# Kernel optimization log

Measured on AMD Instinct MI355X. Metric: run time of the kernel, lower is better.

The kernel has to match this reference:

```python
import jax, jax.numpy as jnp
import numpy as np

D_MODEL = 192
DEPTH = 12
D_INNER = 2 * D_MODEL          # 384
D_STATE = 16
D_CONV = 4
DT_RANK = (D_MODEL + 15) // 16  # 12
T_FRAMES = 8
PATCH = 16
IMG = 224
BATCH = 2
NUM_CLASSES = 1000
EPS = 1e-5


def setup_inputs() -> dict:
    key = jax.random.key(0)
    it = iter(jax.random.split(key, 64))
    def rn(shape, s=0.02):
        return jax.random.normal(next(it), shape, jnp.float32) * s
    inp = {
        'x': jax.random.normal(next(it), (BATCH, 3, T_FRAMES, IMG, IMG), jnp.float32),
        'patch_w': rn((D_MODEL, 3, PATCH, PATCH)),
        'patch_b': jnp.zeros((D_MODEL,), jnp.float32),
        'cls_token': rn((1, 1, D_MODEL)),
        'pos_embed': rn((1, (IMG // PATCH) ** 2 + 1, D_MODEL)),
        'temporal_pos': rn((1, T_FRAMES, D_MODEL)),
        'norm_w': jnp.ones((DEPTH, D_MODEL), jnp.float32),
        'in_proj_w': rn((DEPTH, 2 * D_INNER, D_MODEL)),
        'out_proj_w': rn((DEPTH, D_MODEL, D_INNER)),
        'norm_f_w': jnp.ones((D_MODEL,), jnp.float32),
        'head_w': rn((NUM_CLASSES, D_MODEL)),
        'head_b': jnp.zeros((NUM_CLASSES,), jnp.float32),
    }
    for sfx in ('f', 'b'):  # forward / backward scan direction params (bimamba)
        inp['conv_w_' + sfx] = rn((DEPTH, D_INNER, D_CONV), 0.3)
        inp['conv_b_' + sfx] = jnp.zeros((DEPTH, D_INNER), jnp.float32)
        inp['xproj_w_' + sfx] = rn((DEPTH, DT_RANK + 2 * D_STATE, D_INNER))
        inp['dtproj_w_' + sfx] = rn((DEPTH, D_INNER, DT_RANK), DT_RANK ** -0.5)
        dtv = jnp.exp(jax.random.uniform(next(it), (DEPTH, D_INNER))
                      * (np.log(0.1) - np.log(0.001)) + np.log(0.001))
        inp['dtproj_b_' + sfx] = jnp.log(jnp.expm1(dtv))  # inverse softplus init
        inp['A_log_' + sfx] = jnp.log(jnp.broadcast_to(
            jnp.arange(1, D_STATE + 1, dtype=jnp.float32), (DEPTH, D_INNER, D_STATE)))
        inp['D_' + sfx] = jnp.ones((DEPTH, D_INNER), jnp.float32)
    return inp


def _rmsnorm(x, w):
    return x * jax.lax.rsqrt(jnp.mean(x * x, -1, keepdims=True) + EPS) * w


def _causal_conv(x, w, b):
    # x: [B,L,di], depthwise causal conv along L, kernel D_CONV
    xT = jnp.swapaxes(x, 1, 2)  # [B,di,L]
    y = jax.lax.conv_general_dilated(
        xT, w[:, None, :], (1,), [(D_CONV - 1, 0)],
        feature_group_count=D_INNER, dimension_numbers=('NCH', 'OIH', 'NCH'))
    return jnp.swapaxes(y + b[None, :, None], 1, 2)


def _selective_scan(u, dt, A, Bm, Cm, Dp):
    # u, dt: [B,L,di]; Bm, Cm: [B,L,N]; A: [di,N]; Dp: [di]
    def step(h, xs):
        dt_t, B_t, u_t = xs  # [B,di],[B,N],[B,di]
        h = jnp.exp(dt_t[:, :, None] * A) * h + (dt_t * u_t)[:, :, None] * B_t[:, None, :]
        return h, h
    xs = (jnp.swapaxes(dt, 0, 1), jnp.swapaxes(Bm, 0, 1), jnp.swapaxes(u, 0, 1))
    h0 = jnp.zeros((u.shape[0], A.shape[0], A.shape[1]), u.dtype)
    _, hs = jax.lax.scan(step, h0, xs)  # hs: [L,B,di,N]
    return jnp.einsum('lbdn,bln->bld', hs, Cm) + u * Dp


def _mamba_dir(x, z, conv_w, conv_b, xp_w, dtp_w, dtp_b, A_log, Dp):
    xc = jax.nn.silu(_causal_conv(x, conv_w, conv_b))
    dbl = xc @ xp_w.T  # [B,L,dt_rank+2N]
    dt = dbl[..., :DT_RANK]
    Bm = dbl[..., DT_RANK:DT_RANK + D_STATE]
    Cm = dbl[..., DT_RANK + D_STATE:]
    dt = jax.nn.softplus(dt @ dtp_w.T + dtp_b)
    y = _selective_scan(xc, dt, -jnp.exp(A_log), Bm, Cm, Dp)
    return y * jax.nn.silu(z)


def reference(x, patch_w, patch_b, cls_token, pos_embed, temporal_pos,
              norm_w, in_proj_w, out_proj_w, norm_f_w, head_w, head_b,
              conv_w_f, conv_b_f, xproj_w_f, dtproj_w_f, dtproj_b_f, A_log_f, D_f,
              conv_w_b, conv_b_b, xproj_w_b, dtproj_w_b, dtproj_b_b, A_log_b, D_b):
    B_, C, T, H, W = x.shape
    Hp = H // PATCH
    # PatchEmbed: Conv3d kernel (1,P,P) stride (1,P,P) == per-frame patchify matmul
    xr = x.reshape(B_, C, T, Hp, PATCH, Hp, PATCH)
    feat = jnp.einsum('bcthpwq,ecpq->bethw', xr, patch_w) + patch_b[None, :, None, None, None]
    n = Hp * Hp
    seq = feat.transpose(0, 2, 3, 4, 1).reshape(B_ * T, n, D_MODEL)
    cls = jnp.broadcast_to(cls_token, (B_ * T, 1, D_MODEL))
    seq = jnp.concatenate([cls, seq], 1) + pos_embed
    cls_tok = seq[:B_, :1, :]
    spat = seq[:, 1:].reshape(B_, T, n, D_MODEL).transpose(0, 2, 1, 3)  # (b n) t m
    spat = spat + temporal_pos
    spat = spat.transpose(0, 2, 1, 3).reshape(B_, T * n, D_MODEL)  # b (t n) m
    h = jnp.concatenate([cls_tok, spat], 1)  # [B, 1 + T*n, D]

    res = None
    for i in range(DEPTH):
        # fused add + RMSNorm (prenorm): res = h + res; hn = rmsnorm(res)
        res = h if res is None else h + res
        hn = _rmsnorm(res, norm_w[i])
        # bidirectional Mamba mixer
        xz = hn @ in_proj_w[i].T
        xf, zf = jnp.split(xz, 2, -1)
        y_f = _mamba_dir(xf, zf, conv_w_f[i], conv_b_f[i], xproj_w_f[i],
                         dtproj_w_f[i], dtproj_b_f[i], A_log_f[i], D_f[i])
        y_b = _mamba_dir(xf[:, ::-1], zf[:, ::-1], conv_w_b[i], conv_b_b[i], xproj_w_b[i],
                         dtproj_w_b[i], dtproj_b_b[i], A_log_b[i], D_b[i])[:, ::-1]
        h = (y_f + y_b) @ out_proj_w[i].T

    h = _rmsnorm(h + res, norm_f_w)
    return h[:, 0] @ head_w.T + head_b  # cls token -> head: [B, num_classes]
```

## Files before the change

### kernel.cpp

```cpp
#include <hip/hip_runtime.h>
#include <hip/hip_bf16.h>
#include <math.h>

constexpr int B_   = 2;
constexpr int T_   = 8;
constexpr int DM   = 192;
constexpr int DI   = 384;
constexpr int DS   = 16;
constexpr int DTR  = 12;
constexpr int NP   = 196;
constexpr int L_   = 1 + T_*NP;
constexpr int BL   = B_*L_;
constexpr int DEPTH_ = 12;
constexpr int NCLS = 1000;
constexpr int NC   = 128;
constexpr int LC   = 13;
constexpr int GSCAN = 2*B_*NC;
constexpr size_t BLDI = (size_t)BL*DI;

typedef __attribute__((ext_vector_type(8))) short short8;
typedef __attribute__((ext_vector_type(4))) float f32x4;

constexpr int NWI = DEPTH_*768*DM;
constexpr int NWO = DEPTH_*DM*DI;
constexpr int NWP = DM*768;
constexpr int NWX = DEPTH_*2*64*384;

constexpr size_t OFF_RES = 0;
constexpr size_t OFF_HNB = OFF_RES + (size_t)BL*DM;
constexpr size_t OFF_H   = OFF_HNB + (size_t)BL*DM/2;
constexpr size_t OFF_XZ  = OFF_H   + (size_t)BL*DM;
constexpr size_t OFF_XC  = OFF_XZ  + (size_t)BL*384;
constexpr size_t OFF_DBL = OFF_XC  + (size_t)BL*384;
constexpr size_t OFF_YS  = OFF_DBL + (size_t)BL*128;
constexpr size_t OFF_HE  = OFF_YS  + BLDI;
constexpr size_t OFF_SDT = OFF_HE  + (size_t)GSCAN*384*16/2;
constexpr size_t OFF_FR  = OFF_SDT + (size_t)GSCAN*384;
constexpr size_t OFF_WI  = OFF_FR  + 512;
constexpr size_t OFF_WO  = OFF_WI  + (size_t)NWI/2;
constexpr size_t OFF_WP  = OFF_WO  + (size_t)NWO/2;
constexpr size_t OFF_WX  = OFF_WP  + (size_t)NWP/2;
constexpr size_t WS_FLOATS = OFF_WX + (size_t)NWX/2;

#define DEV_INLINE __device__ __forceinline__

DEV_INLINE void load16(const float* __restrict__ p, float* v) {
  const float4* q = (const float4*)p;
  #pragma unroll
  for (int i = 0; i < 4; ++i) {
    float4 t = q[i];
    v[4*i+0]=t.x; v[4*i+1]=t.y; v[4*i+2]=t.z; v[4*i+3]=t.w;
  }
}
DEV_INLINE void load12(const float* __restrict__ p, float* v) {
  const float4* q = (const float4*)p;
  #pragma unroll
  for (int i = 0; i < 3; ++i) {
    float4 t = q[i];
    v[4*i+0]=t.x; v[4*i+1]=t.y; v[4*i+2]=t.z; v[4*i+3]=t.w;
  }
}

DEV_INLINE float silu_f(float x) { return x / (1.f + __expf(-x)); }
DEV_INLINE float bs2f(short s) {
  unsigned u = ((unsigned)(unsigned short)s) << 16;
  float f; __builtin_memcpy(&f, &u, 4); return f;
}
DEV_INLINE short f2bs(float f) {
  __hip_bfloat16 h = __float2bfloat16(f);
  short s; __builtin_memcpy(&s, &h, 2); return s;
}
DEV_INLINE void store_c(float* p, float v) { *p = v; }
DEV_INLINE void store_c(__hip_bfloat16* p, float v) { *p = __float2bfloat16(v); }

DEV_INLINE float dot12(const float* dv, const float* w, float bias) {
  float a = bias, b = 0.f;
  #pragma unroll
  for (int q = 0; q < 6; ++q) a = fmaf(dv[q], w[q], a);
  #pragma unroll
  for (int q = 6; q < 12; ++q) b = fmaf(dv[q], w[q], b);
  return a + b;
}
DEV_INLINE void powtree(float g, float* G) {
  G[0] = g; G[1] = g*g; G[2] = G[1]*g; G[3] = G[1]*G[1];
  #pragma unroll
  for (int s = 0; s < 4; ++s) G[4+s] = G[3]*G[s];
  #pragma unroll
  for (int s = 0; s < 8; ++s) G[8+s] = G[7]*G[s];
}

__global__ __launch_bounds__(256) void wcast_k(
// ... 56 lines not shown
      float4 x1 = *(const float4*)(xp + 4);
      short8 v;
      v[0]=f2bs(x0.x); v[1]=f2bs(x0.y); v[2]=f2bs(x0.z); v[3]=f2bs(x0.w);
      v[4]=f2bs(x1.x); v[5]=f2bs(x1.y); v[6]=f2bs(x1.z); v[7]=f2bs(x1.w);
      *(short8*)&Als[r*32 + ((gs ^ ((r>>1)&3))*8)] = v;
    }
    {
      int r = lr;
      short8 v = *(const short8*)(Wp + (size_t)(bn + r)*768 + k0 + gs*8);
      *(short8*)&Bls[r*32 + ((gs ^ ((r>>1)&3))*8)] = v;
    }
    __syncthreads();
    short8 af[4], bfq[2];
    #pragma unroll
    for (int mf = 0; mf < 4; ++mf) {
      int r = wm*64 + mf*16 + (lane & 15);
      int kg = (lane >> 4) ^ ((r >> 1) & 3);
      af[mf] = *(const short8*)&Als[r*32 + kg*8];
    }
    #pragma unroll
    for (int nf = 0; nf < 2; ++nf) {
      int r = wn*32 + nf*16 + (lane & 15);
      int kg = (lane >> 4) ^ ((r >> 1) & 3);
      bfq[nf] = *(const short8*)&Bls[r*32 + kg*8];
    }
    #pragma unroll
    for (int mf = 0; mf < 4; ++mf)
      #pragma unroll
      for (int nf = 0; nf < 2; ++nf)
        acc[mf][nf] = __builtin_amdgcn_mfma_f32_16x16x32_bf16(af[mf], bfq[nf], acc[mf][nf], 0, 0, 0);
    __syncthreads();
  }
  int cr0 = (lane >> 4) * 4;
  int cc  = lane & 15;
  #pragma unroll
  for (int mf = 0; mf < 4; ++mf) {
    #pragma unroll
    for (int nf = 0; nf < 2; ++nf) {
      int col = bn + wn*32 + nf*16 + cc;
      #pragma unroll
      for (int r = 0; r < 4; ++r) {
        int row = bm + wm*64 + mf*16 + cr0 + r;
        if (row >= 3136) continue;
        int rem = row % 1568; int bb = row / 1568;
        int t = rem / NP, p = rem % NP;
        size_t orow = (size_t)bb*L_ + 1 + rem;
        float add = epb[col] + eppos[(size_t)(1+p)*DM + col] + eptpos[(size_t)t*DM + col];
        h[orow*DM + col] = acc[mf][nf][r] + add;
      }
    }
  }
}

template <int BM, typename OutT>
__global__ __launch_bounds__(256) void gemm_k(
    const __hip_bfloat16* __restrict__ A_, const __hip_bfloat16* __restrict__ W_,
    OutT* __restrict__ C, int M, int N, int K, int lda, int ldw, int ldc) {
  constexpr int MF = BM/32;
  __shared__ short Als[BM*32];
  __shared__ short Bls[64*32];
  const short* Ap = (const short*)A_;
  const short* Wp = (const short*)W_;
  int bm = blockIdx.x * BM;
  int bn = blockIdx.y * 64;
  int tid = threadIdx.x;
  int lane = tid & 63, wid = tid >> 6;
  int wm = wid & 1, wn = wid >> 1;
  f32x4 acc[MF][2];
  #pragma unroll
  for (int mf = 0; mf < MF; ++mf)
    #pragma unroll
    for (int nf = 0; nf < 2; ++nf) acc[mf][nf] = {0.f,0.f,0.f,0.f};

  int lr = tid >> 2;
  int gs = tid & 3;

  for (int k0 = 0; k0 < K; k0 += 32) {
    #pragma unroll
    for (int hh = 0; hh < BM/64; ++hh) {
      int r = lr + hh*64;
      int gr = bm + r; if (gr >= M) gr = M - 1;
      short8 v = *(const short8*)(Ap + (size_t)gr*lda + k0 + gs*8);
      *(short8*)&Als[r*32 + ((gs ^ ((r>>1)&3))*8)] = v;
    }
    {
      int r = lr;
      short8 v = *(const short8*)(Wp + (size_t)(bn + r)*ldw + k0 + gs*8);
      *(short8*)&Bls[r*32 + ((gs ^ ((r>>1)&3))*8)] = v;
    }
    __syncthreads();
    short8 af[MF], bfq[2];
    #pragma unroll
    for (int mf = 0; mf < MF; ++mf) {
      int r = wm*(BM/2) + mf*16 + (lane & 15);
      int kg = (lane >> 4) ^ ((r >> 1) & 3);
      af[mf] = *(const short8*)&Als[r*32 + kg*8];
    }
    #pragma unroll
    for (int nf = 0; nf < 2; ++nf) {
      int r = wn*32 + nf*16 + (lane & 15);
      int kg = (lane >> 4) ^ ((r >> 1) & 3);
      bfq[nf] = *(const short8*)&Bls[r*32 + kg*8];
    }
    #pragma unroll
    for (int mf = 0; mf < MF; ++mf)
      #pragma unroll
      for (int nf = 0; nf < 2; ++nf)
        acc[mf][nf] = __builtin_amdgcn_mfma_f32_16x16x32_bf16(af[mf], bfq[nf], acc[mf][nf], 0, 0, 0);
    __syncthreads();
  }
  int cr0 = (lane >> 4) * 4;
  int cc  = lane & 15;
  #pragma unroll
  for (int mf = 0; mf < MF; ++mf) {
    #pragma unroll
    for (int nf = 0; nf < 2; ++nf) {
      int col = bn + wn*32 + nf*16 + cc;
      #pragma unroll
      for (int r = 0; r < 4; ++r) {
        int row = bm + wm*(BM/2) + mf*16 + cr0 + r;
        if (row < M) store_c(&C[(size_t)row*ldc + col], acc[mf][nf][r]);
      }
    }
  }
}

__global__ __launch_bounds__(256) void gemm_xc_k(
    const __hip_bfloat16* __restrict__ xz_, const __hip_bfloat16* __restrict__ wx_,
    const float* __restrict__ cwf, const float* __restrict__ cbf,
    const float* __restrict__ cwb, const float* __restrict__ cbb,
    float* __restrict__ dbl, __hip_bfloat16* __restrict__ xc) {
  __shared__ short Als[32*32];
  __shared__ short Bls[64*32];
  __shared__ float wconv[384*4];
  __shared__ float bconv[384];
  int bm = blockIdx.x*32, dir = blockIdx.y;
  const short* xz = (const short*)xz_;
  const short* Wp = (const short*)wx_ + (size_t)dir*64*384;
  const float* cw = dir ? cwb : cwf;
  const float* cb = dir ? cbb : cbf;
  int tid = threadIdx.x;
  for (int i = tid; i < 384; i += 256) {
    ((float4*)wconv)[i] = ((const float4*)cw)[i];
    bconv[i] = cb[i];
  }
  __syncthreads();
  int lane = tid & 63, wid = tid >> 6;
  int wm = wid & 1, wn = wid >> 1;
  f32x4 acc[2] = {{0.f,0.f,0.f,0.f},{0.f,0.f,0.f,0.f}};
  int lr = tid >> 2, gs = tid & 3;

  for (int k0 = 0; k0 < 384; k0 += 32) {
    if (tid < 128) {
      int r = tid >> 2, g2 = tid & 3;
      int gr = bm + r; if (gr >= BL) gr = BL - 1;
      int l = gr % L_, b = gr / L_;
      int d0 = k0 + g2*8;
      float accv[8];
      #pragma unroll
      for (int j = 0; j < 8; ++j) accv[j] = bconv[d0+j];
      const short* base = xz + (size_t)b*L_*768 + d0;
      #pragma unroll
      for (int k = 0; k < 4; ++k) {
        int lsrc = l - 3 + k;
        if (lsrc < 0) continue;
        int lorig = dir ? (L_-1-lsrc) : lsrc;
        short8 xv = *(const short8*)(base + (size_t)lorig*768);
        #pragma unroll
        for (int j = 0; j < 8; ++j)
          accv[j] = fmaf(bs2f(xv[j]), wconv[(d0+j)*4 + k], accv[j]);
      }
      short8 v;
      #pragma unroll
      for (int j = 0; j < 8; ++j) v[j] = f2bs(silu_f(accv[j]));
      *(short8*)&Als[r*32 + ((g2 ^ ((r>>1)&3))*8)] = v;
      *(short8*)((short*)xc + (size_t)gr*768 + dir*384 + d0) = v;
    }
    {
      int r = lr;
      short8 v = *(const short8*)(Wp + (size_t)r*384 + k0 + gs*8);
      *(short8*)&Bls[r*32 + ((gs ^ ((r>>1)&3))*8)] = v;
    }
    __syncthreads();
    short8 af;
    {
      int r = wm*16 + (lane & 15);
      int kg = (lane >> 4) ^ ((r >> 1) & 3);
      af = *(const short8*)&Als[r*32 + kg*8];
    }
    short8 bfq[2];
    #pragma unroll
    for (int nf = 0; nf < 2; ++nf) {
      int r = wn*32 + nf*16 + (lane & 15);
      int kg = (lane >> 4) ^ ((r >> 1) & 3);
      bfq[nf] = *(const short8*)&Bls[r*32 + kg*8];
    }
    #pragma unroll
    for (int nf = 0; nf < 2; ++nf)
      acc[nf] = __builtin_amdgcn_mfma_f32_16x16x32_bf16(af, bfq[nf], acc[nf], 0, 0, 0);
    __syncthreads();
  }
  int cr0 = (lane >> 4) * 4;
  int cc  = lane & 15;
  #pragma unroll
  for (int nf = 0; nf < 2; ++nf) {
    int col = wn*32 + nf*16 + cc;
    #pragma unroll
    for (int r = 0; r < 4; ++r) {
      int row = bm + wm*16 + cr0 + r;
      if (row < BL) dbl[(size_t)row*128 + dir*64 + col] = acc[nf][r];
    }
  }
}

__global__ __launch_bounds__(64) void rmsnorm_res_k(
    const float* __restrict__ h, float* __restrict__ res,
    __hip_bfloat16* __restrict__ hn, const float* __restrict__ w,
    const float* __restrict__ cls, const float* __restrict__ pos) {
  size_t row = blockIdx.x;
  int t = threadIdx.x;
  int l = (int)(row % L_);
  const float* hr = h + row*DM;
  float* rr = res + row*DM;
  float v[3];
  float ss = 0.f;
  #pragma unroll
  for (int i = 0; i < 3; ++i) {
    int e = t + i*64;
    float xv = (l == 0) ? (cls[e] + pos[e]) : hr[e];
    v[i] = xv;
    ss += xv*xv;
  }
  #pragma unroll
  for (int off = 32; off; off >>= 1) ss += __shfl_xor(ss, off);
  float sc = rsqrtf(ss * (1.f/DM) + 1e-5f);
  #pragma unroll
  for (int i = 0; i < 3; ++i) {
    int e = t + i*64;
    rr[e] = v[i];
    hn[row*DM + e] = __float2bfloat16(v[i] * sc * w[e]);
  }
}

__global__ __launch_bounds__(384) void scanA_k(
    const __hip_bfloat16* __restrict__ xc, const float* __restrict__ dbl,
    const float* __restrict__ dtw_f, const float* __restrict__ dtb_f,
    const float* __restrict__ dtw_b, const float* __restrict__ dtb_b,
    const float* __restrict__ dp_f, const float* __restrict__ dp_b,
    __hip_bfloat16* __restrict__ ys, __hip_bfloat16* __restrict__ hend,
    float* __restrict__ sdt) {
  int blk = blockIdx.x;
  int c = blk & (NC-1);
  int rb = blk >> 7;
  int b = rb & 1, dir = rb >> 1;
  int d = threadIdx.x;
  float wdt[DTR];
  load12((dir ? dtw_b : dtw_f) + (size_t)d*DTR, wdt);
  float bdt = (dir ? dtb_b : dtb_f)[d];
  float Dd  = (dir ? dp_b : dp_f)[d];
  const short* xcp = (const short*)xc;
  short* ysp = (short*)ys + (size_t)dir*BLDI;
  float hs[DS];
  #pragma unroll
  for (int s = 0; s < DS; ++s) hs[s] = 0.f;
  float sumdt = 0.f;
  int l0 = c*LC;
  #pragma unroll
  for (int j = 0; j < LC; ++j) {
    int l = l0 + j;
    bool ok = (l < L_);
    size_t row = (size_t)b*L_ + (ok ? l : (L_-1));
    const float* dr = dbl + row*128 + dir*64;
    float dv[DTR];
    load12(dr, dv);
    float a0 = dot12(dv, wdt, bdt);
    float t = __expf(a0);
    float dtv = (a0 > 15.f) ? a0 : __logf(1.f + t);
    float g = __builtin_amdgcn_rcpf(1.f + t);
    if (!ok) { dtv = 0.f; g = 1.f; }
    float u = bs2f(xcp[row*768 + dir*384 + d]);
    float Bv[DS], Cv[DS];
    load16(dr + DTR, Bv);
    load16(dr + DTR + DS, Cv);
    sumdt += dtv;
    float du = dtv*u;
    float G[DS];
    powtree(g, G);
    float p0 = 0.f, p1 = 0.f, p2 = 0.f, p3 = 0.f;
    #pragma unroll
    for (int s = 0; s < DS; s += 4) {
      hs[s+0] = fmaf(G[s+0], hs[s+0], du*Bv[s+0]);
      hs[s+1] = fmaf(G[s+1], hs[s+1], du*Bv[s+1]);
      hs[s+2] = fmaf(G[s+2], hs[s+2], du*Bv[s+2]);
// ... 82 lines not shown
  int d = threadIdx.x;
  size_t hbase = (((size_t)rb*NC + c)*384 + d)*16;
  const short* hp = (const short*)hend;
  float ci[DS];
  {
    short8 h0 = *(const short8*)(hp + hbase);
    short8 h1 = *(const short8*)(hp + hbase + 8);
    #pragma unroll
    for (int s = 0; s < 8; ++s) { ci[s] = bs2f(h0[s]); ci[s+8] = bs2f(h1[s]); }
  }
  float wdt[DTR];
  load12((dir ? dtw_b : dtw_f) + (size_t)d*DTR, wdt);
  float bdt = (dir ? dtb_b : dtb_f)[d];
  short* ysp = (short*)ys + (size_t)dir*BLDI;
  float gj[LC];
  #pragma unroll
  for (int j = 0; j < LC; ++j) {
    int l = l0 + j;
    size_t row = (size_t)b*L_ + ((l < L_) ? l : (L_-1));
    const float* dr = dbl + row*128 + dir*64;
    float dv[DTR];
    load12(dr, dv);
    float a0 = dot12(dv, wdt, bdt);
    gj[j] = (l < L_) ? __builtin_amdgcn_rcpf(1.f + __expf(a0)) : 1.f;
  }
  float qc[LC];
  {
    float p = 1.f;
    #pragma unroll
    for (int j = 0; j < LC; ++j) { p *= gj[j]; qc[j] = p; }
  }
  #pragma unroll
  for (int j = 0; j < LC; ++j) {
    int l = l0 + j;
    if (l >= L_) break;
    size_t row = (size_t)b*L_ + l;
    float Cv[DS];
    load16(dbl + row*128 + dir*64 + DTR + DS, Cv);
    float G[DS];
    powtree(qc[j], G);
    float p0 = 0.f, p1 = 0.f, p2 = 0.f, p3 = 0.f;
    #pragma unroll
    for (int s = 0; s < DS; s += 4) {
      p0 = fmaf(G[s+0]*ci[s+0], Cv[s+0], p0);
      p1 = fmaf(G[s+1]*ci[s+1], Cv[s+1], p1);
      p2 = fmaf(G[s+2]*ci[s+2], Cv[s+2], p2);
      p3 = fmaf(G[s+3]*ci[s+3], Cv[s+3], p3);
    }
    size_t idx = row*DI + d;
    ysp[idx] = f2bs(bs2f(ysp[idx]) + ((p0+p1)+(p2+p3)));
  }
}

template <int WANT_XZ>
__global__ __launch_bounds__(256) void gemm_out_k(
    const __hip_bfloat16* __restrict__ xz_, const __hip_bfloat16* __restrict__ ys_,
    const __hip_bfloat16* __restrict__ W_, float* __restrict__ res,
    const float* __restrict__ nw, const __hip_bfloat16* __restrict__ wi_next,
    __hip_bfloat16* __restrict__ xz_next) {
  constexpr int M = BL;
  __shared__ __align__(16) short Als[16*32];
  __shared__ __align__(16) short Bls[192*32];
  __shared__ float etile[16][194];
  __shared__ __align__(16) short hnls[16*200];
  __shared__ __align__(16) short Bls2[64*200];
  __shared__ float nwls[192];
  const short* xz = (const short*)xz_;
  const short* ysb = (const short*)ys_;
  const short* Wp = (const short*)W_;
  int bm = blockIdx.x * 16;
  int tid = threadIdx.x;
  int lane = tid & 63, wid = tid >> 6;
  f32x4 acc[3];
  #pragma unroll
  for (int nf = 0; nf < 3; ++nf) acc[nf] = {0.f,0.f,0.f,0.f};

  if (WANT_XZ) {
    for (int i = tid; i < 192; i += 256) nwls[i] = nw[i];
  }

  for (int k0 = 0; k0 < 384; k0 += 32) {
    if (tid < 64) {
      int r = tid >> 2, gs = tid & 3;
      int gr = bm + r; if (gr >= M) gr = M - 1;
      int l = gr % L_, b = gr / L_;
      int kk = k0 + gs*8;
      short8 zv = *(const short8*)(xz + (size_t)gr*768 + 384 + kk);
      short8 yf = *(const short8*)(ysb + (size_t)gr*384 + kk);
      short8 yb = *(const short8*)(ysb + BLDI + ((size_t)b*L_ + (L_-1-l))*384 + kk);
      short8 v;
      #pragma unroll
      for (int j = 0; j < 8; ++j)
        v[j] = f2bs(silu_f(bs2f(zv[j])) * (bs2f(yf[j]) + bs2f(yb[j])));
      *(short8*)&Als[r*32 + ((gs ^ ((r>>1)&3))*8)] = v;
    }
    {
      int r0 = tid >> 2, gs = tid & 3;
      #pragma unroll
      for (int hh = 0; hh < 3; ++hh) {
        int r = r0 + hh*64;
        short8 v = *(const short8*)(Wp + (size_t)r*384 + k0 + gs*8);
        *(short8*)&Bls[r*32 + ((gs ^ ((r>>1)&3))*8)] = v;
      }
    }
    __syncthreads();
    short8 af;
    {
      int r = lane & 15;
      int kg = (lane >> 4) ^ ((r >> 1) & 3);
      af = *(const short8*)&Als[r*32 + kg*8];
    }
    short8 bfq[3];
    #pragma unroll
    for (int nf = 0; nf < 3; ++nf) {
      int r = wid*48 + nf*16 + (lane & 15);
      int kg = (lane >> 4) ^ ((r >> 1) & 3);
      bfq[nf] = *(const short8*)&Bls[r*32 + kg*8];
    }
    #pragma unroll
    for (int nf = 0; nf < 3; ++nf)
      acc[nf] = __builtin_amdgcn_mfma_f32_16x16x32_bf16(af, bfq[nf], acc[nf], 0, 0, 0);
    __syncthreads();
  }
  int cr0 = (lane >> 4) * 4;
  int cc  = lane & 15;
  #pragma unroll
  for (int nf = 0; nf < 3; ++nf) {
    int col = wid*48 + nf*16 + cc;
    #pragma unroll
    for (int r = 0; r < 4; ++r) {
      int rl = cr0 + r;
      int grow = bm + rl;
      float v = acc[nf][r];
      if (grow < M) {
        v += res[(size_t)grow*DM + col];
        res[(size_t)grow*DM + col] = v;
      }
      etile[rl][col] = v;
    }
  }
  __syncthreads();

  if (!WANT_XZ) return;

  {
    int row = tid >> 4, part = tid & 15;
    float vals[12];
    float ss = 0.f;
    #pragma unroll
    for (int j = 0; j < 12; ++j) {
      float v = etile[row][part*12 + j];
      vals[j] = v;
      ss += v*v;
    }
    ss += __shfl_xor(ss, 1);
    ss += __shfl_xor(ss, 2);
    ss += __shfl_xor(ss, 4);
    ss += __shfl_xor(ss, 8);
    float sc = rsqrtf(ss * (1.f/DM) + 1e-5f);
    #pragma unroll
    for (int j = 0; j < 12; ++j) {
      int k = part*12 + j;
      int sg = ((k >> 3) & 3) ^ ((row >> 1) & 3);
      hnls[row*200 + (k & ~31) + sg*8 + (k & 7)] =
          f2bs(vals[j] * sc * nwls[k]);
    }
  }
  __syncthreads();

  const short* wip = (const short*)wi_next;
  for (int nt = 0; nt < 12; ++nt) {
    #pragma unroll
    for (int u = 0; u < 6; ++u) {
      int idx = tid + u*256;
      int r = idx / 24, g = idx % 24;
      int k8 = g*8;
      int sg = ((k8 >> 3) & 3) ^ ((r >> 1) & 3);
      short8 v = *(const short8*)(wip + (size_t)(nt*64 + r)*192 + k8);
      *(short8*)&Bls2[r*200 + (k8 & ~31) + sg*8] = v;
    }
    __syncthreads();
    f32x4 acc2 = {0.f,0.f,0.f,0.f};
    #pragma unroll
    for (int k0 = 0; k0 < 192; k0 += 32) {
      int rA = lane & 15;
      int kgA = (lane >> 4) ^ ((rA >> 1) & 3);
      short8 af = *(const short8*)&hnls[rA*200 + k0 + kgA*8];
      int rB = wid*16 + (lane & 15);
      int kgB = (lane >> 4) ^ ((rB >> 1) & 3);
      short8 bf = *(const short8*)&Bls2[rB*200 + k0 + kgB*8];
      acc2 = __builtin_amdgcn_mfma_f32_16x16x32_bf16(af, bf, acc2, 0, 0, 0);
    }
    #pragma unroll
    for (int r = 0; r < 4; ++r) {
      int grow = bm + cr0 + r;
      if (grow < M)
        xz_next[(size_t)grow*768 + nt*64 + wid*16 + cc] = __float2bfloat16(acc2[r]);
    }
    __syncthreads();
  }
}

__global__ __launch_bounds__(256) void head_k(
    const float* __restrict__ res, const float* __restrict__ nf,
    const float* __restrict__ hw, const float* __restrict__ hb,
    float* __restrict__ out) {
  __shared__ __align__(16) float frow[2][192];
  int tid = threadIdx.x;
  int wv = tid >> 6;
  if (wv < 2) {
    int t = tid & 63;
    const float* rr = res + (size_t)wv*L_*DM;
    float v[3]; float ss = 0.f;
    #pragma unroll
    for (int i = 0; i < 3; ++i) {
      int e = t + i*64;
      float xv = rr[e];
      v[i] = xv; ss += xv*xv;
    }
    #pragma unroll
    for (int off = 32; off; off >>= 1) ss += __shfl_xor(ss, off);
    float sc = rsqrtf(ss * (1.f/DM) + 1e-5f);
    #pragma unroll
    for (int i = 0; i < 3; ++i) {
      int e = t + i*64;
      frow[wv][e] = v[i]*sc*nf[e];
    }
  }
  __syncthreads();
  int gid = blockIdx.x*256 + tid;
  if (gid >= B_*NCLS) return;
  int cls = gid % NCLS; int b = gid / NCLS;
  const float4* f4 = (const float4*)frow[b];
  const float4* w4 = (const float4*)(hw + (size_t)cls*DM);
  float acc = hb[cls];
  #pragma unroll
  for (int i = 0; i < DM/4; ++i) {
    float4 a = f4[i], w = w4[i];
    acc += a.x*w.x + a.y*w.y + a.z*w.z + a.w*w.w;
  }
  out[gid] = acc;
}

extern "C" void kernel_launch(void* const* d_in, const int* in_sizes, int n_in,
                              void* d_out, int out_size, void* d_ws, size_t ws_size,
                              hipStream_t stream) {
  const float* x        = (const float*)d_in[0];
  const float* patch_w  = (const float*)d_in[1];
  const float* patch_b  = (const float*)d_in[2];
  const float* cls_tok  = (const float*)d_in[3];
  const float* pos_emb  = (const float*)d_in[4];
  const float* temp_pos = (const float*)d_in[5];
  const float* norm_w   = (const float*)d_in[6];
  const float* in_proj  = (const float*)d_in[7];
  const float* out_proj = (const float*)d_in[8];
  const float* norm_f   = (const float*)d_in[9];
  const float* head_w   = (const float*)d_in[10];
  const float* head_b   = (const float*)d_in[11];
  const float* conv_w_f = (const float*)d_in[12];
  const float* conv_b_f = (const float*)d_in[13];
  const float* xpw_f    = (const float*)d_in[14];
  const float* dtw_f    = (const float*)d_in[15];
  const float* dtb_f    = (const float*)d_in[16];
  const float* alog_f   = (const float*)d_in[17];
  const float* dp_f     = (const float*)d_in[18];
  const float* conv_w_b = (const float*)d_in[19];
  const float* conv_b_b = (const float*)d_in[20];
  const float* xpw_b    = (const float*)d_in[21];
  const float* dtw_b    = (const float*)d_in[22];
  const float* dtb_b    = (const float*)d_in[23];
  const float* alog_b   = (const float*)d_in[24];
  const float* dp_b     = (const float*)d_in[25];
  (void)alog_f; (void)alog_b;

  if (ws_size < WS_FLOATS * sizeof(float)) return;

  float* ws  = (float*)d_ws;
  float* res = ws + OFF_RES;
  __hip_bfloat16* hnb = (__hip_bfloat16*)(ws + OFF_HNB);
  float* h   = ws + OFF_H;
  __hip_bfloat16* xz  = (__hip_bfloat16*)(ws + OFF_XZ);
  __hip_bfloat16* xc  = (__hip_bfloat16*)(ws + OFF_XC);
  float* dbl = ws + OFF_DBL;
  __hip_bfloat16* ys  = (__hip_bfloat16*)(ws + OFF_YS);
  __hip_bfloat16* hend = (__hip_bfloat16*)(ws + OFF_HE);
  float* sdt = ws + OFF_SDT;
  __hip_bfloat16* wi = (__hip_bfloat16*)(ws + OFF_WI);
  __hip_bfloat16* wo = (__hip_bfloat16*)(ws + OFF_WO);
  __hip_bfloat16* wp = (__hip_bfloat16*)(ws + OFF_WP);
  __hip_bfloat16* wx = (__hip_bfloat16*)(ws + OFF_WX);

  {
    int tot = NWI + NWO + NWP + NWX;
    wcast_k<<<dim3((tot + 255)/256), dim3(256), 0, stream>>>(
        in_proj, out_proj, patch_w, xpw_f, xpw_b, wi, wo, wp, wx);
  }

  gemm_patch_k<<<dim3(25, 3), dim3(256), 0, stream>>>(
      x, wp, h, patch_b, pos_emb, temp_pos);

  rmsnorm_res_k<<<dim3(BL), dim3(64), 0, stream>>>(
      h, res, hnb, norm_w, cls_tok, pos_emb);

  const int gM128 = (BL + 127) / 128;
  const int gM32  = (BL + 31) / 32;
  const int gOut  = (BL + 15) / 16;

  gemm_k<128,__hip_bfloat16><<<dim3(gM128, 768/64), dim3(256), 0, stream>>>(
      hnb, wi, xz, BL, 768, DM, DM, DM, 768);

  for (int i = 0; i < DEPTH_; ++i) {
    gemm_xc_k<<<dim3(gM32, 2), dim3(256), 0, stream>>>(
        xz, wx + (size_t)i*2*64*384,
        conv_w_f + (size_t)i*DI*4, conv_b_f + (size_t)i*DI,
        conv_w_b + (size_t)i*DI*4, conv_b_b + (size_t)i*DI,
        dbl, xc);

    const float* adtwf = dtw_f + (size_t)i*DI*DTR;
    const float* adtbf = dtb_f + (size_t)i*DI;
    const float* adtwb = dtw_b + (size_t)i*DI*DTR;
    const float* adtbb = dtb_b + (size_t)i*DI;
    const float* adpf  = dp_f + (size_t)i*DI;
    const float* adpb  = dp_b + (size_t)i*DI;

    scanA_k<<<dim3(GSCAN), dim3(384), 0, stream>>>(
        xc, dbl, adtwf, adtbf, adtwb, adtbb, adpf, adpb, ys, hend, sdt);
    scanB_k<<<dim3(384), dim3(256), 0, stream>>>(hend, sdt);
    scanC_k<<<dim3(GSCAN), dim3(384), 0, stream>>>(
        dbl, hend, adtwf, adtbf, adtwb, adtbb, ys);

    if (i < DEPTH_-1) {
      gemm_out_k<1><<<dim3(gOut), dim3(256), 0, stream>>>(
          xz, ys, wo + (size_t)i*DM*DI, res,
          norm_w + (size_t)(i+1)*DM, wi + (size_t)(i+1)*768*DM, xz);
    } else {
      gemm_out_k<0><<<dim3(gOut), dim3(256), 0, stream>>>(
          xz, ys, wo + (size_t)i*DM*DI, res, nullptr, nullptr, nullptr);
    }
  }

  head_k<<<dim3((B_*NCLS + 255)/256), dim3(256), 0, stream>>>(
      res, norm_f, head_w, head_b, (float*)d_out);
}
```

Measured before the change: 1.008 ms.

## Fuse initial RMSNorm into first in_proj GEMM and final norm+head into last out_proj

Replaces the separate rmsnorm_res kernel and the first in_proj GEMM with one pre_k kernel. It normalizes a 16-row tile into shared memory and multiplies it against all 768 in_proj columns, so the bf16 normalized buffer no longer goes through global memory. The final out_proj kernel now applies the final RMSNorm and the classifier head in the blocks holding the CLS rows, which removes head_k and the final res writeback. The cost is two fewer launches in exchange for less parallel first-layer GEMM tiles, and the head work is serialized into just two blocks.

```diff
diff --git a/kernel.cpp b/kernel.cpp
--- a/kernel.cpp
+++ b/kernel.cpp
@@ -27,16 +27,14 @@
 constexpr int NWX = DEPTH_*2*64*384;
 
 constexpr size_t OFF_RES = 0;
-constexpr size_t OFF_HNB = OFF_RES + (size_t)BL*DM;
-constexpr size_t OFF_H   = OFF_HNB + (size_t)BL*DM/2;
+constexpr size_t OFF_H   = OFF_RES + (size_t)BL*DM;
 constexpr size_t OFF_XZ  = OFF_H   + (size_t)BL*DM;
 constexpr size_t OFF_XC  = OFF_XZ  + (size_t)BL*384;
 constexpr size_t OFF_DBL = OFF_XC  + (size_t)BL*384;
 constexpr size_t OFF_YS  = OFF_DBL + (size_t)BL*128;
 constexpr size_t OFF_HE  = OFF_YS  + BLDI;
 constexpr size_t OFF_SDT = OFF_HE  + (size_t)GSCAN*384*16/2;
-constexpr size_t OFF_FR  = OFF_SDT + (size_t)GSCAN*384;
-constexpr size_t OFF_WI  = OFF_FR  + 512;
+constexpr size_t OFF_WI  = OFF_SDT + (size_t)GSCAN*384;
 constexpr size_t OFF_WO  = OFF_WI  + (size_t)NWI/2;
 constexpr size_t OFF_WP  = OFF_WO  + (size_t)NWO/2;
 constexpr size_t OFF_WX  = OFF_WP  + (size_t)NWP/2;
@@ -199,76 +197,85 @@
   }
 }
 
-template <int BM, typename OutT>
-__global__ __launch_bounds__(256) void gemm_k(
-    const __hip_bfloat16* __restrict__ A_, const __hip_bfloat16* __restrict__ W_,
-    OutT* __restrict__ C, int M, int N, int K, int lda, int ldw, int ldc) {
-  constexpr int MF = BM/32;
-  __shared__ short Als[BM*32];
-  __shared__ short Bls[64*32];
-  const short* Ap = (const short*)A_;
-  const short* Wp = (const short*)W_;
-  int bm = blockIdx.x * BM;
-  int bn = blockIdx.y * 64;
+__global__ __launch_bounds__(256) void pre_k(
+    const float* __restrict__ h, const float* __restrict__ cls,
+    const float* __restrict__ pos, float* __restrict__ res,
+    const float* __restrict__ nw, const __hip_bfloat16* __restrict__ wi0,
+    __hip_bfloat16* __restrict__ xz) {
+  __shared__ __align__(16) short hnls[16*200];
+  __shared__ __align__(16) short Bls2[64*200];
+  __shared__ float nwls[192];
+  int bm = blockIdx.x * 16;
   int tid = threadIdx.x;
   int lane = tid & 63, wid = tid >> 6;
-  int wm = wid & 1, wn = wid >> 1;
-  f32x4 acc[MF][2];
-  #pragma unroll
-  for (int mf = 0; mf < MF; ++mf)
-    #pragma unroll
-    for (int nf = 0; nf < 2; ++nf) acc[mf][nf] = {0.f,0.f,0.f,0.f};
-
-  int lr = tid >> 2;
-  int gs = tid & 3;
-
-  for (int k0 = 0; k0 < K; k0 += 32) {
-    #pragma unroll
-    for (int hh = 0; hh < BM/64; ++hh) {
-      int r = lr + hh*64;
-      int gr = bm + r; if (gr >= M) gr = M - 1;
-      short8 v = *(const short8*)(Ap + (size_t)gr*lda + k0 + gs*8);
-      *(short8*)&Als[r*32 + ((gs ^ ((r>>1)&3))*8)] = v;
-    }
-    {
-      int r = lr;
-      short8 v = *(const short8*)(Wp + (size_t)(bn + r)*ldw + k0 + gs*8);
-      *(short8*)&Bls[r*32 + ((gs ^ ((r>>1)&3))*8)] = v;
-    }
-    __syncthreads();
-    short8 af[MF], bfq[2];
-    #pragma unroll
-    for (int mf = 0; mf < MF; ++mf) {
-      int r = wm*(BM/2) + mf*16 + (lane & 15);
-      int kg = (lane >> 4) ^ ((r >> 1) & 3);
-      af[mf] = *(const short8*)&Als[r*32 + kg*8];
-    }
-    #pragma unroll
-    for (int nf = 0; nf < 2; ++nf) {
-      int r = wn*32 + nf*16 + (lane & 15);
-      int kg = (lane >> 4) ^ ((r >> 1) & 3);
-      bfq[nf] = *(const short8*)&Bls[r*32 + kg*8];
-    }
-    #pragma unroll
-    for (int mf = 0; mf < MF; ++mf)
-      #pragma unroll
-      for (int nf = 0; nf < 2; ++nf)
-        acc[mf][nf] = __builtin_amdgcn_mfma_f32_16x16x32_bf16(af[mf], bfq[nf], acc[mf][nf], 0, 0, 0);
-    __syncthreads();
-  }
+  for (int i = tid; i < 192; i += 256) nwls[i] = nw[i];
+  {
+    int row = tid >> 4, part = tid & 15;
+    int grow = bm + row;
+    bool ok = grow < BL;
+    int gc = ok ? grow : BL - 1;
+    int l = gc % L_;
+    float vals[12];
+    float ss = 0.f;
+    #pragma unroll
+    for (int j = 0; j < 12; ++j) {
+      int e = part*12 + j;
+      float xv = (l == 0) ? (cls[e] + pos[e]) : h[(size_t)gc*DM + e];
+      vals[j] = xv;
+      ss += xv*xv;
+    }
+    ss += __shfl_xor(ss, 1);
+    ss += __shfl_xor(ss, 2);
+    ss += __shfl_xor(ss, 4);
+    ss += __shfl_xor(ss, 8);
+    float sc = rsqrtf(ss * (1.f/DM) + 1e-5f);
+    if (ok) {
+      #pragma unroll
+      for (int j = 0; j < 12; ++j)
+        res[(size_t)grow*DM + part*12 + j] = vals[j];
+    }
+    __syncthreads();
+    #pragma unroll
+    for (int j = 0; j < 12; ++j) {
+      int k = part*12 + j;
+      int sg = ((k >> 3) & 3) ^ ((row >> 1) & 3);
+      hnls[row*200 + (k & ~31) + sg*8 + (k & 7)] =
+          f2bs(vals[j] * sc * nwls[k]);
+    }
+  }
+  __syncthreads();
   int cr0 = (lane >> 4) * 4;
   int cc  = lane & 15;
-  #pragma unroll
-  for (int mf = 0; mf < MF; ++mf) {
-    #pragma unroll
-    for (int nf = 0; nf < 2; ++nf) {
-      int col = bn + wn*32 + nf*16 + cc;
-      #pragma unroll
-      for (int r = 0; r < 4; ++r) {
-        int row = bm + wm*(BM/2) + mf*16 + cr0 + r;
-        if (row < M) store_c(&C[(size_t)row*ldc + col], acc[mf][nf][r]);
-      }
-    }
+  const short* wip = (const short*)wi0;
+  for (int nt = 0; nt < 12; ++nt) {
+    #pragma unroll
+    for (int u = 0; u < 6; ++u) {
+      int idx = tid + u*256;
+      int r = idx / 24, g = idx % 24;
+      int k8 = g*8;
+      int sg = ((k8 >> 3) & 3) ^ ((r >> 1) & 3);
+      short8 v = *(const short8*)(wip + (size_t)(nt*64 + r)*192 + k8);
+      *(short8*)&Bls2[r*200 + (k8 & ~31) + sg*8] = v;
+    }
+    __syncthreads();
+    f32x4 acc2 = {0.f,0.f,0.f,0.f};
+    #pragma unroll
+    for (int k0 = 0; k0 < 192; k0 += 32) {
+      int rA = lane & 15;
+      int kgA = (lane >> 4) ^ ((rA >> 1) & 3);
+      short8 af = *(const short8*)&hnls[rA*200 + k0 + kgA*8];
+      int rB = wid*16 + (lane & 15);
+      int kgB = (lane >> 4) ^ ((rB >> 1) & 3);
+      short8 bf = *(const short8*)&Bls2[rB*200 + k0 + kgB*8];
+      acc2 = __builtin_amdgcn_mfma_f32_16x16x32_bf16(af, bf, acc2, 0, 0, 0);
+    }
+    #pragma unroll
+    for (int r = 0; r < 4; ++r) {
+      int grow = bm + cr0 + r;
+      if (grow < BL)
+        xz[(size_t)grow*768 + nt*64 + wid*16 + cc] = __float2bfloat16(acc2[r]);
+    }
+    __syncthreads();
   }
 }
 
@@ -357,35 +364,6 @@
       int row = bm + wm*16 + cr0 + r;
       if (row < BL) dbl[(size_t)row*128 + dir*64 + col] = acc[nf][r];
     }
-  }
-}
-
-__global__ __launch_bounds__(64) void rmsnorm_res_k(
-    const float* __restrict__ h, float* __restrict__ res,
-    __hip_bfloat16* __restrict__ hn, const float* __restrict__ w,
-    const float* __restrict__ cls, const float* __restrict__ pos) {
-  size_t row = blockIdx.x;
-  int t = threadIdx.x;
-  int l = (int)(row % L_);
-  const float* hr = h + row*DM;
-  float* rr = res + row*DM;
-  float v[3];
-  float ss = 0.f;
-  #pragma unroll
-  for (int i = 0; i < 3; ++i) {
-    int e = t + i*64;
-    float xv = (l == 0) ? (cls[e] + pos[e]) : hr[e];
-    v[i] = xv;
-    ss += xv*xv;
-  }
-  #pragma unroll
-  for (int off = 32; off; off >>= 1) ss += __shfl_xor(ss, off);
-  float sc = rsqrtf(ss * (1.f/DM) + 1e-5f);
-  #pragma unroll
-  for (int i = 0; i < 3; ++i) {
-    int e = t + i*64;
-    rr[e] = v[i];
-    hn[row*DM + e] = __float2bfloat16(v[i] * sc * w[e]);
   }
 }
 
@@ -574,12 +552,14 @@
   }
 }
 
-template <int WANT_XZ>
+template <int MODE>
 __global__ __launch_bounds__(256) void gemm_out_k(
     const __hip_bfloat16* __restrict__ xz_, const __hip_bfloat16* __restrict__ ys_,
     const __hip_bfloat16* __restrict__ W_, float* __restrict__ res,
     const float* __restrict__ nw, const __hip_bfloat16* __restrict__ wi_next,
-    __hip_bfloat16* __restrict__ xz_next) {
+    __hip_bfloat16* __restrict__ xz_next,
+    const float* __restrict__ nfw, const float* __restrict__ hw,
+    const float* __restrict__ hb, float* __restrict__ out) {
   constexpr int M = BL;
   __shared__ __align__(16) short Als[16*32];
   __shared__ __align__(16) short Bls[192*32];
@@ -597,7 +577,7 @@
   #pragma unroll
   for (int nf = 0; nf < 3; ++nf) acc[nf] = {0.f,0.f,0.f,0.f};
 
-  if (WANT_XZ) {
+  if (MODE == 1) {
     for (int i = tid; i < 192; i += 256) nwls[i] = nw[i];
   }
 
@@ -656,14 +636,50 @@
       float v = acc[nf][r];
       if (grow < M) {
         v += res[(size_t)grow*DM + col];
-        res[(size_t)grow*DM + col] = v;
+        if (MODE == 1) res[(size_t)grow*DM + col] = v;
       }
       etile[rl][col] = v;
     }
   }
   __syncthreads();
 
-  if (!WANT_XZ) return;
+  if (MODE == 0) {
+    int crow = -1, bidx = 0;
+    if (bm == 0) { crow = 0; bidx = 0; }
+    else if (bm <= L_ && L_ < bm + 16) { crow = L_ - bm; bidx = 1; }
+    if (crow < 0) return;
+    __shared__ __align__(16) float fr[192];
+    if (tid < 64) {
+      float v[3]; float ss = 0.f;
+      #pragma unroll
+      for (int i = 0; i < 3; ++i) {
+        int e = tid + i*64;
+        float xv = etile[crow][e];
+        v[i] = xv; ss += xv*xv;
+      }
+      #pragma unroll
+      for (int off = 32; off; off >>= 1) ss += __shfl_xor(ss, off);
+      float sc = rsqrtf(ss * (1.f/DM) + 1e-5f);
+      #pragma unroll
+      for (int i = 0; i < 3; ++i) {
+        int e = tid + i*64;
+        fr[e] = v[i]*sc*nfw[e];
+      }
+    }
+    __syncthreads();
+    for (int cls = tid; cls < NCLS; cls += 256) {
+      const float4* f4 = (const float4*)fr;
+      const float4* w4 = (const float4*)(hw + (size_t)cls*DM);
+      float a = hb[cls];
+      #pragma unroll
+      for (int i = 0; i < DM/4; ++i) {
+        float4 av = f4[i], wv = w4[i];
+        a += av.x*wv.x + av.y*wv.y + av.z*wv.z + av.w*wv.w;
+      }
+      out[bidx*NCLS + cls] = a;
+    }
+    return;
+  }
 
   {
     int row = tid >> 4, part = tid & 15;
@@ -721,47 +737,6 @@
     }
     __syncthreads();
   }
-}
-
-__global__ __launch_bounds__(256) void head_k(
-    const float* __restrict__ res, const float* __restrict__ nf,
-    const float* __restrict__ hw, const float* __restrict__ hb,
-    float* __restrict__ out) {
-  __shared__ __align__(16) float frow[2][192];
-  int tid = threadIdx.x;
-  int wv = tid >> 6;
-  if (wv < 2) {
-    int t = tid & 63;
-    const float* rr = res + (size_t)wv*L_*DM;
-    float v[3]; float ss = 0.f;
-    #pragma unroll
-    for (int i = 0; i < 3; ++i) {
-      int e = t + i*64;
-      float xv = rr[e];
-      v[i] = xv; ss += xv*xv;
-    }
-    #pragma unroll
-    for (int off = 32; off; off >>= 1) ss += __shfl_xor(ss, off);
-    float sc = rsqrtf(ss * (1.f/DM) + 1e-5f);
-    #pragma unroll
-    for (int i = 0; i < 3; ++i) {
-      int e = t + i*64;
-      frow[wv][e] = v[i]*sc*nf[e];
-    }
-  }
-  __syncthreads();
-  int gid = blockIdx.x*256 + tid;
-  if (gid >= B_*NCLS) return;
-  int cls = gid % NCLS; int b = gid / NCLS;
-  const float4* f4 = (const float4*)frow[b];
-  const float4* w4 = (const float4*)(hw + (size_t)cls*DM);
-  float acc = hb[cls];
-  #pragma unroll
-  for (int i = 0; i < DM/4; ++i) {
-    float4 a = f4[i], w = w4[i];
-    acc += a.x*w.x + a.y*w.y + a.z*w.z + a.w*w.w;
-  }
-  out[gid] = acc;
 }
 
 extern "C" void kernel_launch(void* const* d_in, const int* in_sizes, int n_in,
@@ -799,7 +774,6 @@
 
   float* ws  = (float*)d_ws;
   float* res = ws + OFF_RES;
-  __hip_bfloat16* hnb = (__hip_bfloat16*)(ws + OFF_HNB);
   float* h   = ws + OFF_H;
   __hip_bfloat16* xz  = (__hip_bfloat16*)(ws + OFF_XZ);
   __hip_bfloat16* xc  = (__hip_bfloat16*)(ws + OFF_XC);
@@ -821,15 +795,11 @@
   gemm_patch_k<<<dim3(25, 3), dim3(256), 0, stream>>>(
       x, wp, h, patch_b, pos_emb, temp_pos);
 
-  rmsnorm_res_k<<<dim3(BL), dim3(64), 0, stream>>>(
-      h, res, hnb, norm_w, cls_tok, pos_emb);
-
-  const int gM128 = (BL + 127) / 128;
+  const int gOut  = (BL + 15) / 16;
   const int gM32  = (BL + 31) / 32;
-  const int gOut  = (BL + 15) / 16;
-
-  gemm_k<128,__hip_bfloat16><<<dim3(gM128, 768/64), dim3(256), 0, stream>>>(
-      hnb, wi, xz, BL, 768, DM, DM, DM, 768);
+
+  pre_k<<<dim3(gOut), dim3(256), 0, stream>>>(
+      h, cls_tok, pos_emb, res, norm_w, wi, xz);
 
   for (int i = 0; i < DEPTH_; ++i) {
     gemm_xc_k<<<dim3(gM32, 2), dim3(256), 0, stream>>>(
@@ -854,13 +824,13 @@
     if (i < DEPTH_-1) {
       gemm_out_k<1><<<dim3(gOut), dim3(256), 0, stream>>>(
           xz, ys, wo + (size_t)i*DM*DI, res,
-          norm_w + (size_t)(i+1)*DM, wi + (size_t)(i+1)*768*DM, xz);
+          norm_w + (size_t)(i+1)*DM, wi + (size_t)(i+1)*768*DM, xz,
+          nullptr, nullptr, nullptr, nullptr);
     } else {
       gemm_out_k<0><<<dim3(gOut), dim3(256), 0, stream>>>(
-          xz, ys, wo + (size_t)i*DM*DI, res, nullptr, nullptr, nullptr);
-    }
-  }
-
-  head_k<<<dim3((B_*NCLS + 255)/256), dim3(256), 0, stream>>>(
-      res, norm_f, head_w, head_b, (float*)d_out);
-}
+          xz, ys, wo + (size_t)i*DM*DI, res,
+          nullptr, nullptr, nullptr,
+          norm_f, head_w, head_b, (float*)d_out);
+    }
+  }
+}
```

After: 1.010 ms. Within noise of the previous version (+0.2%).

## Unfuse out-proj, RMSNorm and next in-proj into separate tiled kernels

Applied to the files above, without the earlier changes.

Replaces the fused gemm_out kernel (out-projection, residual add, RMSNorm and the next layer's in-projection over 16-row tiles) with three launches. These are a 64x64-tiled out-projection GEMM with a 2D grid, a standalone 4-rows-per-block RMSNorm, and the existing 128-row in-projection GEMM. The fused kernel ran only about 197 blocks of mostly serial work with heavy shared memory, so the split aims for better parallelism and occupancy. In exchange it adds extra launches and a round trip through global memory for res and hnb each layer.

```diff
diff --git a/kernel.cpp b/kernel.cpp
--- a/kernel.cpp
+++ b/kernel.cpp
@@ -35,8 +35,7 @@
 constexpr size_t OFF_YS  = OFF_DBL + (size_t)BL*128;
 constexpr size_t OFF_HE  = OFF_YS  + BLDI;
 constexpr size_t OFF_SDT = OFF_HE  + (size_t)GSCAN*384*16/2;
-constexpr size_t OFF_FR  = OFF_SDT + (size_t)GSCAN*384;
-constexpr size_t OFF_WI  = OFF_FR  + 512;
+constexpr size_t OFF_WI  = OFF_SDT + (size_t)GSCAN*384;
 constexpr size_t OFF_WO  = OFF_WI  + (size_t)NWI/2;
 constexpr size_t OFF_WP  = OFF_WO  + (size_t)NWO/2;
 constexpr size_t OFF_WX  = OFF_WP  + (size_t)NWP/2;
@@ -360,23 +359,23 @@
   }
 }
 
-__global__ __launch_bounds__(64) void rmsnorm_res_k(
-    const float* __restrict__ h, float* __restrict__ res,
+template <int FIRST>
+__global__ __launch_bounds__(256) void rmsn_k(
+    const float* __restrict__ src, float* __restrict__ res,
     __hip_bfloat16* __restrict__ hn, const float* __restrict__ w,
     const float* __restrict__ cls, const float* __restrict__ pos) {
-  size_t row = blockIdx.x;
-  int t = threadIdx.x;
-  int l = (int)(row % L_);
-  const float* hr = h + row*DM;
-  float* rr = res + row*DM;
-  float v[3];
-  float ss = 0.f;
+  int row = blockIdx.x*4 + (threadIdx.x >> 6);
+  if (row >= BL) return;
+  int t = threadIdx.x & 63;
+  float v[3]; float ss = 0.f;
+  int l = row % L_;
   #pragma unroll
   for (int i = 0; i < 3; ++i) {
     int e = t + i*64;
-    float xv = (l == 0) ? (cls[e] + pos[e]) : hr[e];
-    v[i] = xv;
-    ss += xv*xv;
+    float xv;
+    if (FIRST) xv = (l == 0) ? (cls[e] + pos[e]) : src[(size_t)row*DM + e];
+    else       xv = src[(size_t)row*DM + e];
+    v[i] = xv; ss += xv*xv;
   }
   #pragma unroll
   for (int off = 32; off; off >>= 1) ss += __shfl_xor(ss, off);
@@ -384,8 +383,8 @@
   #pragma unroll
   for (int i = 0; i < 3; ++i) {
     int e = t + i*64;
-    rr[e] = v[i];
-    hn[row*DM + e] = __float2bfloat16(v[i] * sc * w[e]);
+    if (FIRST) res[(size_t)row*DM + e] = v[i];
+    hn[(size_t)row*DM + e] = __float2bfloat16(v[i] * sc * w[e]);
   }
 }
 
@@ -574,37 +573,30 @@
   }
 }
 
-template <int WANT_XZ>
-__global__ __launch_bounds__(256) void gemm_out_k(
+__global__ __launch_bounds__(256) void gemm_og_k(
     const __hip_bfloat16* __restrict__ xz_, const __hip_bfloat16* __restrict__ ys_,
-    const __hip_bfloat16* __restrict__ W_, float* __restrict__ res,
-    const float* __restrict__ nw, const __hip_bfloat16* __restrict__ wi_next,
-    __hip_bfloat16* __restrict__ xz_next) {
-  constexpr int M = BL;
-  __shared__ __align__(16) short Als[16*32];
-  __shared__ __align__(16) short Bls[192*32];
-  __shared__ float etile[16][194];
-  __shared__ __align__(16) short hnls[16*200];
-  __shared__ __align__(16) short Bls2[64*200];
-  __shared__ float nwls[192];
+    const __hip_bfloat16* __restrict__ W_, float* __restrict__ res) {
+  __shared__ short Als[64*32];
+  __shared__ short Bls[64*32];
   const short* xz = (const short*)xz_;
   const short* ysb = (const short*)ys_;
   const short* Wp = (const short*)W_;
-  int bm = blockIdx.x * 16;
+  int bm = blockIdx.x * 64;
+  int bn = blockIdx.y * 64;
   int tid = threadIdx.x;
   int lane = tid & 63, wid = tid >> 6;
-  f32x4 acc[3];
-  #pragma unroll
-  for (int nf = 0; nf < 3; ++nf) acc[nf] = {0.f,0.f,0.f,0.f};
-
-  if (WANT_XZ) {
-    for (int i = tid; i < 192; i += 256) nwls[i] = nw[i];
-  }
+  int wm = wid & 1, wn = wid >> 1;
+  f32x4 acc[2][2];
+  #pragma unroll
+  for (int mf = 0; mf < 2; ++mf)
+    #pragma unroll
+    for (int nf = 0; nf < 2; ++nf) acc[mf][nf] = {0.f,0.f,0.f,0.f};
+  int lr = tid >> 2, gs = tid & 3;
 
   for (int k0 = 0; k0 < 384; k0 += 32) {
-    if (tid < 64) {
-      int r = tid >> 2, gs = tid & 3;
-      int gr = bm + r; if (gr >= M) gr = M - 1;
+    {
+      int r = lr;
+      int gr = bm + r; if (gr >= BL) gr = BL - 1;
       int l = gr % L_, b = gr / L_;
       int kk = k0 + gs*8;
       short8 zv = *(const short8*)(xz + (size_t)gr*768 + 384 + kk);
@@ -617,109 +609,47 @@
       *(short8*)&Als[r*32 + ((gs ^ ((r>>1)&3))*8)] = v;
     }
     {
-      int r0 = tid >> 2, gs = tid & 3;
-      #pragma unroll
-      for (int hh = 0; hh < 3; ++hh) {
-        int r = r0 + hh*64;
-        short8 v = *(const short8*)(Wp + (size_t)r*384 + k0 + gs*8);
-        *(short8*)&Bls[r*32 + ((gs ^ ((r>>1)&3))*8)] = v;
-      }
+      int r = lr;
+      short8 v = *(const short8*)(Wp + (size_t)(bn + r)*384 + k0 + gs*8);
+      *(short8*)&Bls[r*32 + ((gs ^ ((r>>1)&3))*8)] = v;
     }
     __syncthreads();
-    short8 af;
-    {
-      int r = lane & 15;
+    short8 af[2], bfq[2];
+    #pragma unroll
+    for (int mf = 0; mf < 2; ++mf) {
+      int r = wm*32 + mf*16 + (lane & 15);
       int kg = (lane >> 4) ^ ((r >> 1) & 3);
-      af = *(const short8*)&Als[r*32 + kg*8];
-    }
-    short8 bfq[3];
-    #pragma unroll
-    for (int nf = 0; nf < 3; ++nf) {
-      int r = wid*48 + nf*16 + (lane & 15);
+      af[mf] = *(const short8*)&Als[r*32 + kg*8];
+    }
+    #pragma unroll
+    for (int nf = 0; nf < 2; ++nf) {
+      int r = wn*32 + nf*16 + (lane & 15);
       int kg = (lane >> 4) ^ ((r >> 1) & 3);
       bfq[nf] = *(const short8*)&Bls[r*32 + kg*8];
     }
     #pragma unroll
-    for (int nf = 0; nf < 3; ++nf)
-      acc[nf] = __builtin_amdgcn_mfma_f32_16x16x32_bf16(af, bfq[nf], acc[nf], 0, 0, 0);
+    for (int mf = 0; mf < 2; ++mf)
+      #pragma unroll
+      for (int nf = 0; nf < 2; ++nf)
+        acc[mf][nf] = __builtin_amdgcn_mfma_f32_16x16x32_bf16(af[mf], bfq[nf], acc[mf][nf], 0, 0, 0);
     __syncthreads();
   }
   int cr0 = (lane >> 4) * 4;
   int cc  = lane & 15;
   #pragma unroll
-  for (int nf = 0; nf < 3; ++nf) {
-    int col = wid*48 + nf*16 + cc;
-    #pragma unroll
-    for (int r = 0; r < 4; ++r) {
-      int rl = cr0 + r;
-      int grow = bm + rl;
-      float v = acc[nf][r];
-      if (grow < M) {
-        v += res[(size_t)grow*DM + col];
-        res[(size_t)grow*DM + col] = v;
+  for (int mf = 0; mf < 2; ++mf) {
+    #pragma unroll
+    for (int nf = 0; nf < 2; ++nf) {
+      int col = bn + wn*32 + nf*16 + cc;
+      #pragma unroll
+      for (int r = 0; r < 4; ++r) {
+        int row = bm + wm*32 + mf*16 + cr0 + r;
+        if (row < BL && col < DM) {
+          size_t idx = (size_t)row*DM + col;
+          res[idx] += acc[mf][nf][r];
+        }
       }
-      etile[rl][col] = v;
-    }
-  }
-  __syncthreads();
-
-  if (!WANT_XZ) return;
-
-  {
-    int row = tid >> 4, part = tid & 15;
-    float vals[12];
-    float ss = 0.f;
-    #pragma unroll
-    for (int j = 0; j < 12; ++j) {
-      float v = etile[row][part*12 + j];
-      vals[j] = v;
-      ss += v*v;
-    }
-    ss += __shfl_xor(ss, 1);
-    ss += __shfl_xor(ss, 2);
-    ss += __shfl_xor(ss, 4);
-    ss += __shfl_xor(ss, 8);
-    float sc = rsqrtf(ss * (1.f/DM) + 1e-5f);
-    #pragma unroll
-    for (int j = 0; j < 12; ++j) {
-      int k = part*12 + j;
-      int sg = ((k >> 3) & 3) ^ ((row >> 1) & 3);
-      hnls[row*200 + (k & ~31) + sg*8 + (k & 7)] =
-          f2bs(vals[j] * sc * nwls[k]);
-    }
-  }
-  __syncthreads();
-
-  const short* wip = (const short*)wi_next;
-  for (int nt = 0; nt < 12; ++nt) {
-    #pragma unroll
-    for (int u = 0; u < 6; ++u) {
-      int idx = tid + u*256;
-      int r = idx / 24, g = idx % 24;
-      int k8 = g*8;
-      int sg = ((k8 >> 3) & 3) ^ ((r >> 1) & 3);
-      short8 v = *(const short8*)(wip + (size_t)(nt*64 + r)*192 + k8);
-      *(short8*)&Bls2[r*200 + (k8 & ~31) + sg*8] = v;
-    }
-    __syncthreads();
-    f32x4 acc2 = {0.f,0.f,0.f,0.f};
-    #pragma unroll
-    for (int k0 = 0; k0 < 192; k0 += 32) {
-      int rA = lane & 15;
-      int kgA = (lane >> 4) ^ ((rA >> 1) & 3);
-      short8 af = *(const short8*)&hnls[rA*200 + k0 + kgA*8];
-      int rB = wid*16 + (lane & 15);
-      int kgB = (lane >> 4) ^ ((rB >> 1) & 3);
-      short8 bf = *(const short8*)&Bls2[rB*200 + k0 + kgB*8];
-      acc2 = __builtin_amdgcn_mfma_f32_16x16x32_bf16(af, bf, acc2, 0, 0, 0);
-    }
-    #pragma unroll
-    for (int r = 0; r < 4; ++r) {
-      int grow = bm + cr0 + r;
-      if (grow < M)
-        xz_next[(size_t)grow*768 + nt*64 + wid*16 + cc] = __float2bfloat16(acc2[r]);
-    }
-    __syncthreads();
+    }
   }
 }
 
@@ -821,14 +751,13 @@
   gemm_patch_k<<<dim3(25, 3), dim3(256), 0, stream>>>(
       x, wp, h, patch_b, pos_emb, temp_pos);
 
-  rmsnorm_res_k<<<dim3(BL), dim3(64), 0, stream>>>(
+  const int gRms = (BL + 3) / 4;
+  const int gM32 = (BL + 31) / 32;
+  const int gOg  = (BL + 63) / 64;
+
+  rmsn_k<1><<<dim3(gRms), dim3(256), 0, stream>>>(
       h, res, hnb, norm_w, cls_tok, pos_emb);
-
-  const int gM128 = (BL + 127) / 128;
-  const int gM32  = (BL + 31) / 32;
-  const int gOut  = (BL + 15) / 16;
-
-  gemm_k<128,__hip_bfloat16><<<dim3(gM128, 768/64), dim3(256), 0, stream>>>(
+  gemm_k<128,__hip_bfloat16><<<dim3(25, 12), dim3(256), 0, stream>>>(
       hnb, wi, xz, BL, 768, DM, DM, DM, 768);
 
   for (int i = 0; i < DEPTH_; ++i) {
@@ -851,13 +780,14 @@
     scanC_k<<<dim3(GSCAN), dim3(384), 0, stream>>>(
         dbl, hend, adtwf, adtbf, adtwb, adtbb, ys);
 
+    gemm_og_k<<<dim3(gOg, 3), dim3(256), 0, stream>>>(
+        xz, ys, wo + (size_t)i*DM*DI, res);
+
     if (i < DEPTH_-1) {
-      gemm_out_k<1><<<dim3(gOut), dim3(256), 0, stream>>>(
-          xz, ys, wo + (size_t)i*DM*DI, res,
-          norm_w + (size_t)(i+1)*DM, wi + (size_t)(i+1)*768*DM, xz);
-    } else {
-      gemm_out_k<0><<<dim3(gOut), dim3(256), 0, stream>>>(
-          xz, ys, wo + (size_t)i*DM*DI, res, nullptr, nullptr, nullptr);
+      rmsn_k<0><<<dim3(gRms), dim3(256), 0, stream>>>(
+          res, nullptr, hnb, norm_w + (size_t)(i+1)*DM, nullptr, nullptr);
+      gemm_k<128,__hip_bfloat16><<<dim3(25, 12), dim3(256), 0, stream>>>(
+          hnb, wi + (size_t)(i+1)*768*DM, xz, BL, 768, DM, DM, DM, 768);
     }
   }
 
```

Measured after the change: 977.4 us. 1.03x faster.
